# Optimization experiments

Measured on AMD Instinct MI355X. Metric: run time of the kernel, lower is better.

## Reference

```python
import jax, jax.numpy as jnp
import numpy as np

B, P, ENC, DEC, ATT = 256, 196, 2048, 512, 512


def setup_inputs() -> dict:
    key = jax.random.key(0)
    ks = jax.random.split(key, 8)
    s_enc = 1.0 / np.sqrt(ENC)
    s_dec = 1.0 / np.sqrt(DEC)
    s_att = 1.0 / np.sqrt(ATT)
    return {
        "encoder_out": jax.random.normal(ks[0], (B, P, ENC), jnp.float32),
        "decoder_hidden": jax.random.normal(ks[1], (B, DEC), jnp.float32),
        "W_enc": jax.random.uniform(ks[2], (ENC, ATT), jnp.float32, -s_enc, s_enc),
        "b_enc": jax.random.uniform(ks[3], (ATT,), jnp.float32, -s_enc, s_enc),
        "W_dec": jax.random.uniform(ks[4], (DEC, ATT), jnp.float32, -s_dec, s_dec),
        "b_dec": jax.random.uniform(ks[5], (ATT,), jnp.float32, -s_dec, s_dec),
        "W_full": jax.random.uniform(ks[6], (ATT,), jnp.float32, -s_att, s_att),
        "b_full": jax.random.uniform(ks[7], (), jnp.float32, -s_att, s_att),
    }


def reference(encoder_out, decoder_hidden, W_enc, b_enc, W_dec, b_dec, W_full, b_full):
    # att1: [B, P, ATT]; att2: [B, ATT]
    att1 = jnp.einsum("bpe,ea->bpa", encoder_out, W_enc) + b_enc
    att2 = decoder_hidden @ W_dec + b_dec
    # additive combine + relu + scalar projection -> [B, P]
    att = jnp.einsum("bpa,a->bp", jax.nn.relu(att1 + att2[:, None, :]), W_full) + b_full
    alpha = jax.nn.softmax(att, axis=1)  # softmax over pixels
    context_vector = jnp.einsum("bpe,bp->be", encoder_out, alpha)
    return (context_vector, alpha)
```

## Files before the change

### kernel.cpp

```cpp
#include <hip/hip_runtime.h>
#include <hip/hip_bf16.h>
#include <stdint.h>


using u16x8 = __attribute__((ext_vector_type(8))) unsigned short;
using s16x8 = __attribute__((ext_vector_type(8))) short;
using f32x4 = __attribute__((ext_vector_type(4))) float;

static __device__ __forceinline__ unsigned short f2b(float f) {
  unsigned int u = __builtin_bit_cast(unsigned int, f);
  u = u + 0x7fffu + ((u >> 16) & 1u);
  return (unsigned short)(u >> 16);
}

__global__ __launch_bounds__(256) void transpose_wenc(
    const float* __restrict__ wenc, unsigned short* __restrict__ wencT) {
  __shared__ unsigned short tile[32][34];
  const int t = threadIdx.x;
  const int x = t & 31, y = t >> 5;
  const int kb = blockIdx.x & 63, nb = blockIdx.x >> 6;
  const int k0 = kb << 5, n0 = nb << 5;
#pragma unroll
  for (int i = 0; i < 4; ++i) {
    int kk = y * 4 + i;
    tile[x][kk] = f2b(wenc[(size_t)(k0 + kk) * 512 + n0 + x]);
  }
  __syncthreads();
#pragma unroll
  for (int i = 0; i < 4; ++i) {
    int nn = y * 4 + i;
    wencT[(size_t)(n0 + nn) * 2048 + k0 + x] = tile[nn][x];
  }
}

__global__ __launch_bounds__(256) void comb_kernel(
    const float* __restrict__ dec, const float* __restrict__ wdec,
    const float* __restrict__ bdec, const float* __restrict__ benc,
    float* __restrict__ comb) {
  __shared__ float dec_sh[8][512];
  const int t = threadIdx.x;
  const int b0 = blockIdx.x * 8;
  for (int i = t; i < 8 * 512; i += 256)
    dec_sh[i >> 9][i & 511] = dec[(size_t)b0 * 512 + i];
  __syncthreads();
  const int a0 = 2 * t;
  float bias0 = bdec[a0] + benc[a0];
  float bias1 = bdec[a0 + 1] + benc[a0 + 1];
  float acc0[8], acc1[8];
#pragma unroll
  for (int i = 0; i < 8; ++i) { acc0[i] = bias0; acc1[i] = bias1; }
  for (int e = 0; e < 512; ++e) {
    float2 wv = *(const float2*)&wdec[(size_t)e * 512 + a0];
#pragma unroll
    for (int i = 0; i < 8; ++i) {
      float d = dec_sh[i][e];
      acc0[i] = fmaf(d, wv.x, acc0[i]);
      acc1[i] = fmaf(d, wv.y, acc1[i]);
    }
  }
#pragma unroll
  for (int i = 0; i < 8; ++i) {
    float2 o = make_float2(acc0[i], acc1[i]);
    *(float2*)&comb[(size_t)(b0 + i) * 512 + a0] = o;
  }
}

#define LROW 40

__global__ __launch_bounds__(512, 4) void gemm_att(
    const float* __restrict__ enc, const unsigned short* __restrict__ wencT,
    const float* __restrict__ comb, const float* __restrict__ wfull_g,
    float* __restrict__ att) {
  __shared__ alignas(16) unsigned short Ash[64 * LROW];
  __shared__ alignas(16) unsigned short Bsh[512 * LROW];
  __shared__ float comb_sh[1024];
  __shared__ float wfull_sh[512];
  __shared__ float att_sh[64];

  const int t = threadIdx.x;
  const int l = t & 63;
  const int w = t >> 6;
  const int quad = l >> 4, col = l & 15;
  const int wm = w >> 2, wn = w & 3;
  const int r0 = blockIdx.x * 64;
  const int b0 = r0 / 196;
  const int rsw = (b0 + 1) * 196;
  const int b1 = (b0 + 1 < 256) ? b0 + 1 : 255;

  comb_sh[t] = comb[(size_t)b0 * 512 + t];
  comb_sh[512 + t] = comb[(size_t)b1 * 512 + t];
  wfull_sh[t] = wfull_g[t];
  if (t < 64) att_sh[t] = 0.0f;

  const float* agp = enc + (size_t)(r0 + ((t & 255) >> 2)) * 2048 + (t & 3) * 8;
  unsigned short* alp = &Ash[((t & 255) >> 2) * LROW + (t & 3) * 8];
  const unsigned short* bgp[4];
  unsigned short* blp[4];
#pragma unroll
  for (int j = 0; j < 4; ++j) {
    int c = j * 512 + t;
    int n = c >> 2, kc = c & 3;
    bgp[j] = wencT + (size_t)n * 2048 + kc * 8;
    blp[j] = &Bsh[n * LROW + kc * 8];
  }

  int aoff[2], boff[8];
#pragma unroll
  for (int mt = 0; mt < 2; ++mt) {
    int ml = wm * 32 + mt * 16 + col;
    aoff[mt] = ml * LROW + quad * 8;
  }
#pragma unroll
  for (int nt = 0; nt < 8; ++nt) {
    int nl = wn * 128 + nt * 16 + col;
    boff[nt] = nl * LROW + quad * 8;
  }

  f32x4 acc[2][8];
#pragma unroll
  for (int mt = 0; mt < 2; ++mt)
#pragma unroll
    for (int nt = 0; nt < 8; ++nt) acc[mt][nt] = (f32x4){0.f, 0.f, 0.f, 0.f};

  for (int ks = 0; ks < 64; ++ks) {
    f32x4 a0v, a1v;
    if (t < 256) {
      a0v = *(const f32x4*)agp;
      a1v = *(const f32x4*)(agp + 4);
    }
    u16x8 bv[4];
#pragma unroll
    for (int j = 0; j < 4; ++j) bv[j] = *(const u16x8*)bgp[j];

    __syncthreads();
    if (t < 256) {
      u16x8 av;
      av[0] = f2b(a0v[0]); av[1] = f2b(a0v[1]);
      av[2] = f2b(a0v[2]); av[3] = f2b(a0v[3]);
      av[4] = f2b(a1v[0]); av[5] = f2b(a1v[1]);
      av[6] = f2b(a1v[2]); av[7] = f2b(a1v[3]);
      *(u16x8*)alp = av;
    }
#pragma unroll
    for (int j = 0; j < 4; ++j) *(u16x8*)blp[j] = bv[j];
    __syncthreads();

    s16x8 afr[2];
#pragma unroll
    for (int mt = 0; mt < 2; ++mt) afr[mt] = *(const s16x8*)&Ash[aoff[mt]];
#pragma unroll
    for (int nt = 0; nt < 8; ++nt) {
      s16x8 bfr = *(const s16x8*)&Bsh[boff[nt]];
      acc[0][nt] = __builtin_amdgcn_mfma_f32_16x16x32_bf16(afr[0], bfr, acc[0][nt], 0, 0, 0);
      acc[1][nt] = __builtin_amdgcn_mfma_f32_16x16x32_bf16(afr[1], bfr, acc[1][nt], 0, 0, 0);
    }

    agp += 32;
#pragma unroll
    for (int j = 0; j < 4; ++j) bgp[j] += 32;
  }

  __syncthreads();
#pragma unroll
  for (int mt = 0; mt < 2; ++mt) {
#pragma unroll
    for (int r = 0; r < 4; ++r) {
      int rl = wm * 32 + mt * 16 + quad * 4 + r;
      int cb = ((r0 + rl) >= rsw) ? 512 : 0;
      float s = 0.f;
#pragma unroll
      for (int nt = 0; nt < 8; ++nt) {
        int n = wn * 128 + nt * 16 + col;
        float v = acc[mt][nt][r] + comb_sh[cb + n];
        v = fmaxf(v, 0.f);
        s = fmaf(v, wfull_sh[n], s);
      }
      s += __shfl_xor(s, 1);
      s += __shfl_xor(s, 2);
      s += __shfl_xor(s, 4);
      s += __shfl_xor(s, 8);
      if (col == 0) atomicAdd(&att_sh[rl], s);
    }
  }
  __syncthreads();
  if (t < 64) att[(size_t)r0 + t] = att_sh[t];
}

__global__ __launch_bounds__(256) void softmax_ctx(
    const float* __restrict__ att, const float* __restrict__ enc,
    float* __restrict__ ctx_out, float* __restrict__ alpha_out) {
  const int b = blockIdx.x, t = threadIdx.x;
  __shared__ float red[256];
  __shared__ float alpha_sh[196];

  float v = (t < 196) ? att[(size_t)b * 196 + t] : -1e30f;
  red[t] = v;
  __syncthreads();
  for (int s = 128; s > 0; s >>= 1) {
    if (t < s) red[t] = fmaxf(red[t], red[t + s]);
    __syncthreads();
  }
  float mx = red[0];
  __syncthreads();
  float e = (t < 196) ? __expf(v - mx) : 0.f;
  red[t] = e;
  __syncthreads();
  for (int s = 128; s > 0; s >>= 1) {
    if (t < s) red[t] += red[t + s];
    __syncthreads();
  }
  float a = e / red[0];
  if (t < 196) {
    alpha_sh[t] = a;
    alpha_out[(size_t)b * 196 + t] = a;
  }
  __syncthreads();

  float acc[8] = {0.f, 0.f, 0.f, 0.f, 0.f, 0.f, 0.f, 0.f};
  const float* ep = enc + (size_t)b * 196 * 2048 + t * 8;
#pragma unroll 2
  for (int p = 0; p < 196; ++p) {
    float ap = alpha_sh[p];
    f32x4 e0 = *(const f32x4*)(ep);
    f32x4 e1 = *(const f32x4*)(ep + 4);
    acc[0] = fmaf(ap, e0[0], acc[0]);
    acc[1] = fmaf(ap, e0[1], acc[1]);
    acc[2] = fmaf(ap, e0[2], acc[2]);
    acc[3] = fmaf(ap, e0[3], acc[3]);
    acc[4] = fmaf(ap, e1[0], acc[4]);
    acc[5] = fmaf(ap, e1[1], acc[5]);
    acc[6] = fmaf(ap, e1[2], acc[6]);
    acc[7] = fmaf(ap, e1[3], acc[7]);
    ep += 2048;
  }
  float* op = ctx_out + (size_t)b * 2048 + t * 8;
  *(f32x4*)op = (f32x4){acc[0], acc[1], acc[2], acc[3]};
  *(f32x4*)(op + 4) = (f32x4){acc[4], acc[5], acc[6], acc[7]};
}

extern "C" void kernel_launch(void* const* d_in, const int* in_sizes, int n_in,
                              void* d_out, int out_size, void* d_ws, size_t ws_size,
                              hipStream_t stream) {
  (void)in_sizes; (void)n_in; (void)out_size; (void)ws_size;
  const float* enc   = (const float*)d_in[0];
  const float* dec   = (const float*)d_in[1];
  const float* wenc  = (const float*)d_in[2];
  const float* benc  = (const float*)d_in[3];
  const float* wdec  = (const float*)d_in[4];
  const float* bdec  = (const float*)d_in[5];
  const float* wfull = (const float*)d_in[6];

  unsigned short* wencT = (unsigned short*)d_ws;
  float* comb = (float*)((char*)d_ws + (2u << 20));
  float* att  = (float*)((char*)d_ws + (2u << 20) + (512u << 10));

  float* ctx_out = (float*)d_out;
  float* alpha_out = ctx_out + (size_t)256 * 2048;

  hipLaunchKernelGGL(transpose_wenc, dim3(1024), dim3(256), 0, stream, wenc, wencT);
  hipLaunchKernelGGL(comb_kernel, dim3(32), dim3(256), 0, stream, dec, wdec, bdec, benc, comb);
  hipLaunchKernelGGL(gemm_att, dim3(784), dim3(512), 0, stream, enc, wencT, comb, wfull, att);
  hipLaunchKernelGGL(softmax_ctx, dim3(256), dim3(256), 0, stream, att, enc, ctx_out, alpha_out);
}
```

Baseline: 830.9 us.

## Retile attention GEMM to 128x128 blocks, fuse prep kernels, split softmax context

Merges the weight transpose, decoder projection and att zeroing into one prep launch. The GEMM moves from 64x512 tiles to 128x128 tiles with 256 threads, loads B into LDS directly via global_load_lds with an XOR swizzle, packs bf16 with hardware conversion, and accumulates att with global atomics across the four N-blocks. The softmax/context kernel is split into two column chunks per batch for more parallelism. The enc tensor (fp32) is now re-read and re-converted four times (once per N block), which trades extra bandwidth for smaller tiles and higher occupancy.

```diff
diff --git a/kernel.cpp b/kernel.cpp
--- a/kernel.cpp
+++ b/kernel.cpp
@@ -4,6 +4,7 @@
 
 
 using u16x8 = __attribute__((ext_vector_type(8))) unsigned short;
+using u32x4 = __attribute__((ext_vector_type(4))) unsigned int;
 using s16x8 = __attribute__((ext_vector_type(8))) short;
 using f32x4 = __attribute__((ext_vector_type(4))) float;
 
@@ -12,184 +13,188 @@
   u = u + 0x7fffu + ((u >> 16) & 1u);
   return (unsigned short)(u >> 16);
 }
-
-__global__ __launch_bounds__(256) void transpose_wenc(
-    const float* __restrict__ wenc, unsigned short* __restrict__ wencT) {
-  __shared__ unsigned short tile[32][34];
-  const int t = threadIdx.x;
-  const int x = t & 31, y = t >> 5;
-  const int kb = blockIdx.x & 63, nb = blockIdx.x >> 6;
-  const int k0 = kb << 5, n0 = nb << 5;
-#pragma unroll
-  for (int i = 0; i < 4; ++i) {
-    int kk = y * 4 + i;
-    tile[x][kk] = f2b(wenc[(size_t)(k0 + kk) * 512 + n0 + x]);
-  }
-  __syncthreads();
-#pragma unroll
-  for (int i = 0; i < 4; ++i) {
-    int nn = y * 4 + i;
-    wencT[(size_t)(n0 + nn) * 2048 + k0 + x] = tile[nn][x];
-  }
-}
-
-__global__ __launch_bounds__(256) void comb_kernel(
+static __device__ __forceinline__ unsigned int cvt_pk(float x, float y) {
+  float2 p; p.x = x; p.y = y;
+  __hip_bfloat162 h = __float22bfloat162_rn(p);
+  unsigned int u;
+  __builtin_memcpy(&u, &h, 4);
+  return u;
+}
+
+__global__ __launch_bounds__(256) void prep_kernel(
+    const float* __restrict__ wenc, unsigned short* __restrict__ wencT,
     const float* __restrict__ dec, const float* __restrict__ wdec,
     const float* __restrict__ bdec, const float* __restrict__ benc,
-    float* __restrict__ comb) {
-  __shared__ float dec_sh[8][512];
-  const int t = threadIdx.x;
-  const int b0 = blockIdx.x * 8;
-  for (int i = t; i < 8 * 512; i += 256)
-    dec_sh[i >> 9][i & 511] = dec[(size_t)b0 * 512 + i];
-  __syncthreads();
-  const int a0 = 2 * t;
-  float bias0 = bdec[a0] + benc[a0];
-  float bias1 = bdec[a0 + 1] + benc[a0 + 1];
-  float acc0[8], acc1[8];
-#pragma unroll
-  for (int i = 0; i < 8; ++i) { acc0[i] = bias0; acc1[i] = bias1; }
-  for (int e = 0; e < 512; ++e) {
-    float2 wv = *(const float2*)&wdec[(size_t)e * 512 + a0];
-#pragma unroll
-    for (int i = 0; i < 8; ++i) {
-      float d = dec_sh[i][e];
-      acc0[i] = fmaf(d, wv.x, acc0[i]);
-      acc1[i] = fmaf(d, wv.y, acc1[i]);
-    }
-  }
-#pragma unroll
-  for (int i = 0; i < 8; ++i) {
-    float2 o = make_float2(acc0[i], acc1[i]);
-    *(float2*)&comb[(size_t)(b0 + i) * 512 + a0] = o;
-  }
-}
-
-#define LROW 40
-
-__global__ __launch_bounds__(512, 4) void gemm_att(
+    float* __restrict__ comb, float* __restrict__ att) {
+  const int bid = blockIdx.x, t = threadIdx.x;
+  if (bid < 1024) {
+    __shared__ unsigned short tile[32][34];
+    const int x = t & 31, y = t >> 5;
+    const int kb = bid & 63, nb = bid >> 6;
+    const int k0 = kb << 5, n0 = nb << 5;
+#pragma unroll
+    for (int i = 0; i < 4; ++i) {
+      int kk = y * 4 + i;
+      tile[x][kk] = f2b(wenc[(size_t)(k0 + kk) * 512 + n0 + x]);
+    }
+    __syncthreads();
+#pragma unroll
+    for (int i = 0; i < 4; ++i) {
+      int nn = y * 4 + i;
+      wencT[(size_t)(n0 + nn) * 2048 + k0 + x] = tile[nn][x];
+    }
+  } else if (bid < 1073) {
+    int idx = (bid - 1024) * 1024 + t * 4;
+    *(f32x4*)&att[idx] = (f32x4){0.f, 0.f, 0.f, 0.f};
+  } else {
+    __shared__ float dec_sh[512];
+    const int b = bid - 1073;
+    dec_sh[t] = dec[(size_t)b * 512 + t];
+    dec_sh[256 + t] = dec[(size_t)b * 512 + 256 + t];
+    __syncthreads();
+    const int a0 = 2 * t;
+    float acc0 = bdec[a0] + benc[a0];
+    float acc1 = bdec[a0 + 1] + benc[a0 + 1];
+    for (int e = 0; e < 512; ++e) {
+      float2 wv = *(const float2*)&wdec[(size_t)e * 512 + a0];
+      float d = dec_sh[e];
+      acc0 = fmaf(d, wv.x, acc0);
+      acc1 = fmaf(d, wv.y, acc1);
+    }
+    float2 o; o.x = acc0; o.y = acc1;
+    *(float2*)&comb[(size_t)b * 512 + a0] = o;
+  }
+}
+
+static __device__ __forceinline__ void load_lds16(const unsigned short* g,
+                                                  unsigned short* l) {
+  __builtin_amdgcn_global_load_lds(
+      (const __attribute__((address_space(1))) unsigned int*)g,
+      (__attribute__((address_space(3))) unsigned int*)l, 16, 0, 0);
+}
+
+#define LROWA 40
+
+__global__ __launch_bounds__(256, 3) void gemm_att(
     const float* __restrict__ enc, const unsigned short* __restrict__ wencT,
     const float* __restrict__ comb, const float* __restrict__ wfull_g,
     float* __restrict__ att) {
-  __shared__ alignas(16) unsigned short Ash[64 * LROW];
-  __shared__ alignas(16) unsigned short Bsh[512 * LROW];
-  __shared__ float comb_sh[1024];
-  __shared__ float wfull_sh[512];
-  __shared__ float att_sh[64];
+  __shared__ alignas(16) unsigned short Ash[128 * LROWA];
+  __shared__ alignas(16) unsigned short Bsh[128 * 32];
+  __shared__ float comb_sh[256];
+  __shared__ float wfull_sh[128];
 
   const int t = threadIdx.x;
-  const int l = t & 63;
-  const int w = t >> 6;
+  const int w = t >> 6, l = t & 63;
   const int quad = l >> 4, col = l & 15;
-  const int wm = w >> 2, wn = w & 3;
-  const int r0 = blockIdx.x * 64;
+  const int wm = w >> 1, wn = w & 1;
+  const int mb = blockIdx.x >> 2, nb = blockIdx.x & 3;
+  const int r0 = mb * 128, n0 = nb * 128;
   const int b0 = r0 / 196;
   const int rsw = (b0 + 1) * 196;
   const int b1 = (b0 + 1 < 256) ? b0 + 1 : 255;
 
-  comb_sh[t] = comb[(size_t)b0 * 512 + t];
-  comb_sh[512 + t] = comb[(size_t)b1 * 512 + t];
-  wfull_sh[t] = wfull_g[t];
-  if (t < 64) att_sh[t] = 0.0f;
-
-  const float* agp = enc + (size_t)(r0 + ((t & 255) >> 2)) * 2048 + (t & 3) * 8;
-  unsigned short* alp = &Ash[((t & 255) >> 2) * LROW + (t & 3) * 8];
-  const unsigned short* bgp[4];
-  unsigned short* blp[4];
-#pragma unroll
-  for (int j = 0; j < 4; ++j) {
-    int c = j * 512 + t;
-    int n = c >> 2, kc = c & 3;
-    bgp[j] = wencT + (size_t)n * 2048 + kc * 8;
-    blp[j] = &Bsh[n * LROW + kc * 8];
-  }
-
-  int aoff[2], boff[8];
-#pragma unroll
-  for (int mt = 0; mt < 2; ++mt) {
-    int ml = wm * 32 + mt * 16 + col;
-    aoff[mt] = ml * LROW + quad * 8;
-  }
-#pragma unroll
-  for (int nt = 0; nt < 8; ++nt) {
-    int nl = wn * 128 + nt * 16 + col;
-    boff[nt] = nl * LROW + quad * 8;
-  }
-
-  f32x4 acc[2][8];
-#pragma unroll
-  for (int mt = 0; mt < 2; ++mt)
-#pragma unroll
-    for (int nt = 0; nt < 8; ++nt) acc[mt][nt] = (f32x4){0.f, 0.f, 0.f, 0.f};
+  if (t < 128) {
+    comb_sh[t] = comb[(size_t)b0 * 512 + n0 + t];
+    wfull_sh[t] = wfull_g[n0 + t];
+  } else {
+    comb_sh[t] = comb[(size_t)b1 * 512 + n0 + (t - 128)];
+  }
+
+  const float* agp = enc + (size_t)(r0 + (t >> 1)) * 2048 + (t & 1) * 16;
+  unsigned short* alp = &Ash[(t >> 1) * LROWA + (t & 1) * 16];
+
+  const unsigned short* bgp[2];
+  unsigned short* blp[2];
+#pragma unroll
+  for (int j = 0; j < 2; ++j) {
+    int q = (w * 2 + j) * 64 + l;
+    int n = q >> 2, kc = (q & 3) ^ ((q >> 4) & 3);
+    bgp[j] = wencT + (size_t)(n0 + n) * 2048 + kc * 8;
+    blp[j] = &Bsh[(w * 2 + j) * 512];
+  }
+
+  int aoff[4], boff[4];
+#pragma unroll
+  for (int mt = 0; mt < 4; ++mt)
+    aoff[mt] = (wm * 64 + mt * 16 + col) * LROWA + quad * 8;
+#pragma unroll
+  for (int nt = 0; nt < 4; ++nt) {
+    int nl = wn * 64 + nt * 16 + col;
+    boff[nt] = nl * 32 + (quad ^ ((nl >> 2) & 3)) * 8;
+  }
+
+  f32x4 acc[4][4];
+#pragma unroll
+  for (int mt = 0; mt < 4; ++mt)
+#pragma unroll
+    for (int nt = 0; nt < 4; ++nt) acc[mt][nt] = (f32x4){0.f, 0.f, 0.f, 0.f};
 
   for (int ks = 0; ks < 64; ++ks) {
-    f32x4 a0v, a1v;
-    if (t < 256) {
-      a0v = *(const f32x4*)agp;
-      a1v = *(const f32x4*)(agp + 4);
-    }
-    u16x8 bv[4];
-#pragma unroll
-    for (int j = 0; j < 4; ++j) bv[j] = *(const u16x8*)bgp[j];
-
-    __syncthreads();
-    if (t < 256) {
-      u16x8 av;
-      av[0] = f2b(a0v[0]); av[1] = f2b(a0v[1]);
-      av[2] = f2b(a0v[2]); av[3] = f2b(a0v[3]);
-      av[4] = f2b(a1v[0]); av[5] = f2b(a1v[1]);
-      av[6] = f2b(a1v[2]); av[7] = f2b(a1v[3]);
-      *(u16x8*)alp = av;
-    }
-#pragma unroll
-    for (int j = 0; j < 4; ++j) *(u16x8*)blp[j] = bv[j];
-    __syncthreads();
-
-    s16x8 afr[2];
-#pragma unroll
-    for (int mt = 0; mt < 2; ++mt) afr[mt] = *(const s16x8*)&Ash[aoff[mt]];
-#pragma unroll
-    for (int nt = 0; nt < 8; ++nt) {
+    f32x4 av[4];
+#pragma unroll
+    for (int i = 0; i < 4; ++i) av[i] = *(const f32x4*)(agp + i * 4);
+
+    __syncthreads();
+
+    u32x4 pk0, pk1;
+#pragma unroll
+    for (int i = 0; i < 2; ++i) {
+      pk0[2 * i]     = cvt_pk(av[i][0], av[i][1]);
+      pk0[2 * i + 1] = cvt_pk(av[i][2], av[i][3]);
+      pk1[2 * i]     = cvt_pk(av[i + 2][0], av[i + 2][1]);
+      pk1[2 * i + 1] = cvt_pk(av[i + 2][2], av[i + 2][3]);
+    }
+    *(u32x4*)alp = pk0;
+    *(u32x4*)(alp + 8) = pk1;
+#pragma unroll
+    for (int j = 0; j < 2; ++j) load_lds16(bgp[j], blp[j]);
+
+    __syncthreads();
+
+    s16x8 afr[4];
+#pragma unroll
+    for (int mt = 0; mt < 4; ++mt) afr[mt] = *(const s16x8*)&Ash[aoff[mt]];
+#pragma unroll
+    for (int nt = 0; nt < 4; ++nt) {
       s16x8 bfr = *(const s16x8*)&Bsh[boff[nt]];
-      acc[0][nt] = __builtin_amdgcn_mfma_f32_16x16x32_bf16(afr[0], bfr, acc[0][nt], 0, 0, 0);
-      acc[1][nt] = __builtin_amdgcn_mfma_f32_16x16x32_bf16(afr[1], bfr, acc[1][nt], 0, 0, 0);
+#pragma unroll
+      for (int mt = 0; mt < 4; ++mt)
+        acc[mt][nt] = __builtin_amdgcn_mfma_f32_16x16x32_bf16(afr[mt], bfr, acc[mt][nt], 0, 0, 0);
     }
 
     agp += 32;
 #pragma unroll
-    for (int j = 0; j < 4; ++j) bgp[j] += 32;
-  }
-
-  __syncthreads();
-#pragma unroll
-  for (int mt = 0; mt < 2; ++mt) {
+    for (int j = 0; j < 2; ++j) bgp[j] += 32;
+  }
+
+#pragma unroll
+  for (int mt = 0; mt < 4; ++mt) {
 #pragma unroll
     for (int r = 0; r < 4; ++r) {
-      int rl = wm * 32 + mt * 16 + quad * 4 + r;
-      int cb = ((r0 + rl) >= rsw) ? 512 : 0;
+      int rl = wm * 64 + mt * 16 + quad * 4 + r;
+      int cb = ((r0 + rl) >= rsw) ? 128 : 0;
       float s = 0.f;
 #pragma unroll
-      for (int nt = 0; nt < 8; ++nt) {
-        int n = wn * 128 + nt * 16 + col;
-        float v = acc[mt][nt][r] + comb_sh[cb + n];
+      for (int nt = 0; nt < 4; ++nt) {
+        int nl = wn * 64 + nt * 16 + col;
+        float v = acc[mt][nt][r] + comb_sh[cb + nl];
         v = fmaxf(v, 0.f);
-        s = fmaf(v, wfull_sh[n], s);
+        s = fmaf(v, wfull_sh[nl], s);
       }
       s += __shfl_xor(s, 1);
       s += __shfl_xor(s, 2);
       s += __shfl_xor(s, 4);
       s += __shfl_xor(s, 8);
-      if (col == 0) atomicAdd(&att_sh[rl], s);
-    }
-  }
-  __syncthreads();
-  if (t < 64) att[(size_t)r0 + t] = att_sh[t];
+      if (col == 0) atomicAdd(&att[(size_t)r0 + rl], s);
+    }
+  }
 }
 
 __global__ __launch_bounds__(256) void softmax_ctx(
     const float* __restrict__ att, const float* __restrict__ enc,
     float* __restrict__ ctx_out, float* __restrict__ alpha_out) {
-  const int b = blockIdx.x, t = threadIdx.x;
+  const int b = blockIdx.x, chunk = blockIdx.y, t = threadIdx.x;
   __shared__ float red[256];
   __shared__ float alpha_sh[196];
 
@@ -212,30 +217,23 @@
   float a = e / red[0];
   if (t < 196) {
     alpha_sh[t] = a;
-    alpha_out[(size_t)b * 196 + t] = a;
-  }
-  __syncthreads();
-
-  float acc[8] = {0.f, 0.f, 0.f, 0.f, 0.f, 0.f, 0.f, 0.f};
-  const float* ep = enc + (size_t)b * 196 * 2048 + t * 8;
-#pragma unroll 2
+    if (chunk == 0) alpha_out[(size_t)b * 196 + t] = a;
+  }
+  __syncthreads();
+
+  f32x4 acc = (f32x4){0.f, 0.f, 0.f, 0.f};
+  const float* ep = enc + (size_t)b * 196 * 2048 + chunk * 1024 + t * 4;
+#pragma unroll 4
   for (int p = 0; p < 196; ++p) {
     float ap = alpha_sh[p];
-    f32x4 e0 = *(const f32x4*)(ep);
-    f32x4 e1 = *(const f32x4*)(ep + 4);
-    acc[0] = fmaf(ap, e0[0], acc[0]);
-    acc[1] = fmaf(ap, e0[1], acc[1]);
-    acc[2] = fmaf(ap, e0[2], acc[2]);
-    acc[3] = fmaf(ap, e0[3], acc[3]);
-    acc[4] = fmaf(ap, e1[0], acc[4]);
-    acc[5] = fmaf(ap, e1[1], acc[5]);
-    acc[6] = fmaf(ap, e1[2], acc[6]);
-    acc[7] = fmaf(ap, e1[3], acc[7]);
+    f32x4 ev = *(const f32x4*)ep;
+    acc[0] = fmaf(ap, ev[0], acc[0]);
+    acc[1] = fmaf(ap, ev[1], acc[1]);
+    acc[2] = fmaf(ap, ev[2], acc[2]);
+    acc[3] = fmaf(ap, ev[3], acc[3]);
     ep += 2048;
   }
-  float* op = ctx_out + (size_t)b * 2048 + t * 8;
-  *(f32x4*)op = (f32x4){acc[0], acc[1], acc[2], acc[3]};
-  *(f32x4*)(op + 4) = (f32x4){acc[4], acc[5], acc[6], acc[7]};
+  *(f32x4*)&ctx_out[(size_t)b * 2048 + chunk * 1024 + t * 4] = acc;
 }
 
 extern "C" void kernel_launch(void* const* d_in, const int* in_sizes, int n_in,
@@ -257,8 +255,10 @@
   float* ctx_out = (float*)d_out;
   float* alpha_out = ctx_out + (size_t)256 * 2048;
 
-  hipLaunchKernelGGL(transpose_wenc, dim3(1024), dim3(256), 0, stream, wenc, wencT);
-  hipLaunchKernelGGL(comb_kernel, dim3(32), dim3(256), 0, stream, dec, wdec, bdec, benc, comb);
-  hipLaunchKernelGGL(gemm_att, dim3(784), dim3(512), 0, stream, enc, wencT, comb, wfull, att);
-  hipLaunchKernelGGL(softmax_ctx, dim3(256), dim3(256), 0, stream, att, enc, ctx_out, alpha_out);
-}
+  hipLaunchKernelGGL(prep_kernel, dim3(1329), dim3(256), 0, stream,
+                     wenc, wencT, dec, wdec, bdec, benc, comb, att);
+  hipLaunchKernelGGL(gemm_att, dim3(1568), dim3(256), 0, stream,
+                     enc, wencT, comb, wfull, att);
+  hipLaunchKernelGGL(softmax_ctx, dim3(256, 2), dim3(256), 0, stream,
+                     att, enc, ctx_out, alpha_out);
+}
```

After: 850.2 us. 1.02x slower.
